# Optimization experiments

Measured on AMD Instinct MI355X. Metric: run time of the kernel, lower is better.

## Reference

```python
import jax, jax.numpy as jnp
import numpy as np

B, N, IN_DIM, SLOT_DIM, HIDDEN = 32, 4096, 256, 256, 512
NUM_SLOTS, NUM_ITERS = 8, 3
EPS_LN = 1e-5


def layernorm(x, g, b):
    m = jnp.mean(x, axis=-1, keepdims=True)
    v = jnp.var(x, axis=-1, keepdims=True)
    return (x - m) * jax.lax.rsqrt(v + EPS_LN) * g + b


def setup_inputs() -> dict:
    key = jax.random.key(0)
    ks = jax.random.split(key, 16)
    s = 0.02
    return {
        "inputs": jax.random.normal(ks[0], (B, N, IN_DIM), jnp.float32),
        "init_noise": jax.random.normal(ks[1], (B, NUM_SLOTS, SLOT_DIM), jnp.float32),
        "mu": jax.random.normal(ks[2], (1, 1, SLOT_DIM), jnp.float32),
        "sigma_raw": jax.random.normal(ks[3], (1, 1, SLOT_DIM), jnp.float32),
        "ln_in_g": jnp.ones((IN_DIM,), jnp.float32), "ln_in_b": jnp.zeros((IN_DIM,), jnp.float32),
        "ln_s_g": jnp.ones((SLOT_DIM,), jnp.float32), "ln_s_b": jnp.zeros((SLOT_DIM,), jnp.float32),
        "ln_m_g": jnp.ones((SLOT_DIM,), jnp.float32), "ln_m_b": jnp.zeros((SLOT_DIM,), jnp.float32),
        "wq": jax.random.normal(ks[4], (SLOT_DIM, SLOT_DIM), jnp.float32) * s,
        "bq": jnp.zeros((SLOT_DIM,), jnp.float32),
        "wk": jax.random.normal(ks[5], (SLOT_DIM, IN_DIM), jnp.float32) * s,
        "bk": jnp.zeros((SLOT_DIM,), jnp.float32),
        "wv": jax.random.normal(ks[6], (SLOT_DIM, IN_DIM), jnp.float32) * s,
        "bv": jnp.zeros((SLOT_DIM,), jnp.float32),
        "w_ih": jax.random.normal(ks[7], (3 * SLOT_DIM, SLOT_DIM), jnp.float32) * s,
        "w_hh": jax.random.normal(ks[8], (3 * SLOT_DIM, SLOT_DIM), jnp.float32) * s,
        "b_ih": jnp.zeros((3 * SLOT_DIM,), jnp.float32),
        "b_hh": jnp.zeros((3 * SLOT_DIM,), jnp.float32),
        "w1": jax.random.normal(ks[9], (HIDDEN, SLOT_DIM), jnp.float32) * s,
        "b1": jnp.zeros((HIDDEN,), jnp.float32),
        "w2": jax.random.normal(ks[10], (SLOT_DIM, HIDDEN), jnp.float32) * s,
        "b2": jnp.zeros((SLOT_DIM,), jnp.float32),
    }


def gru_cell(x, h, w_ih, w_hh, b_ih, b_hh):
    # PyTorch GRUCell: gates split as (reset, update, new)
    gx = x @ w_ih.T + b_ih
    gh = h @ w_hh.T + b_hh
    xr, xz, xn = jnp.split(gx, 3, axis=-1)
    hr, hz, hn = jnp.split(gh, 3, axis=-1)
    r = jax.nn.sigmoid(xr + hr)
    z = jax.nn.sigmoid(xz + hz)
    n = jnp.tanh(xn + r * hn)
    return (1.0 - z) * n + z * h


def reference(inputs, init_noise, mu, sigma_raw, ln_in_g, ln_in_b, ln_s_g, ln_s_b,
              ln_m_g, ln_m_b, wq, bq, wk, bk, wv, bv, w_ih, w_hh, b_ih, b_hh,
              w1, b1, w2, b2):
    scale = SLOT_DIM ** (-0.5)
    x = layernorm(inputs, ln_in_g, ln_in_b)          # [B,N,Din]
    k = x @ wk.T + bk                                # [B,N,D]
    v = x @ wv.T + bv                                # [B,N,D]
    sigma = jax.nn.softplus(sigma_raw)
    slots = mu + sigma * init_noise                  # [B,S,D]
    attn = None
    for _ in range(NUM_ITERS):
        slots_prev = slots
        q = layernorm(slots, ln_s_g, ln_s_b) @ wq.T + bq      # [B,S,D]
        logits = jnp.einsum('bnd,bsd->bns', k, q) * scale     # [B,N,S]
        attn = jax.nn.softmax(logits, axis=-1) + 1e-8         # softmax over slots
        attn = attn / jnp.sum(attn, axis=1, keepdims=True)    # renorm over inputs
        updates = jnp.einsum('bnd,bns->bsd', v, attn)         # [B,S,D]
        slots = gru_cell(updates, slots_prev, w_ih, w_hh, b_ih, b_hh)
        h = jax.nn.relu(layernorm(slots, ln_m_g, ln_m_b) @ w1.T + b1)
        slots = slots + (h @ w2.T + b2)
    return slots, attn
```

## Files before the change

kernel.cpp:

```cpp
#include <hip/hip_runtime.h>
#include <hip/hip_fp16.h>
#include <cstdint>

#define DEV static __device__ __forceinline__

typedef _Float16 f16x2 __attribute__((ext_vector_type(2)));
typedef _Float16 f16x8 __attribute__((ext_vector_type(8)));
typedef float    f32x4 __attribute__((ext_vector_type(4)));

DEV float fdot2u(uint32_t a, uint32_t b, float c){
  union U { uint32_t u; f16x2 h; };
  U ua; ua.u = a; U ub; ub.u = b;
#if __has_builtin(__builtin_amdgcn_fdot2)
  return __builtin_amdgcn_fdot2(ua.h, ub.h, c, false);
#else
  return c + (float)ua.h[0]*(float)ub.h[0] + (float)ua.h[1]*(float)ub.h[1];
#endif
}

DEV float dot4(uint4 x, uint4 w, float a){
  a = fdot2u(x.x, w.x, a); a = fdot2u(x.y, w.y, a);
  a = fdot2u(x.z, w.z, a); a = fdot2u(x.w, w.w, a);
  return a;
}

DEV float wsum64(float v){
  #pragma unroll
  for (int o = 32; o; o >>= 1) v += __shfl_xor(v, o);
  return v;
}

DEV uint32_t pack2h(float a, float b){
  __half ha = __float2half(a), hb = __float2half(b);
  return (uint32_t)__half_as_ushort(ha) | ((uint32_t)__half_as_ushort(hb) << 16);
}

DEV uint32_t packsh(float v){
  float o = __shfl_xor(v, 1);
  return pack2h(v, o);
}

DEV uint4 packrow8(const float* p){
  uint4 r;
  r.x = pack2h(p[0], p[1]); r.y = pack2h(p[2], p[3]);
  r.z = pack2h(p[4], p[5]); r.w = pack2h(p[6], p[7]);
  return r;
}

DEV void gld16(const void* g, void* l){
  __builtin_amdgcn_global_load_lds(
      (const __attribute__((address_space(1))) void*)g,
      (__attribute__((address_space(3))) void*)l, 16, 0, 0);
}

__global__ __launch_bounds__(256) void k_lntr(
  const float* __restrict__ xin, const float* __restrict__ lng,
  const float* __restrict__ lnb, uint32_t* __restrict__ xhat,
  const float* __restrict__ wq, const float* __restrict__ wv,
  const float* __restrict__ wih, const float* __restrict__ whh,
  const float* __restrict__ w1, const float* __restrict__ w2,
  const float* __restrict__ wk,
  uint4* __restrict__ WQp4, uint4* __restrict__ WVp4,
  uint4* __restrict__ WIHp4, uint4* __restrict__ WHHp4,
  uint4* __restrict__ W1p4, uint4* __restrict__ W2p4,
  uint4* __restrict__ WKp4)
{
  if (blockIdx.x >= 32768){
    int u = (blockIdx.x - 32768) * 256 + threadIdx.x;
    if (u < 8192){
      int e4 = u >> 8, n = u & 255;
      WVp4[u] = packrow8(wv + n*256 + 8*e4);
    } else if (u < 32768){
      int v = u - 8192; int e4 = v / 768, n = v - e4*768;
      WIHp4[v] = packrow8(wih + n*256 + 8*e4);
    } else if (u < 57344){
      int v = u - 32768; int e4 = v / 768, n = v - e4*768;
      WHHp4[v] = packrow8(whh + n*256 + 8*e4);
    } else if (u < 73728){
      int v = u - 57344; int e4 = v >> 9, n = v & 511;
      W1p4[v] = packrow8(w1 + n*256 + 8*e4);
    } else if (u < 90112){
      int v = u - 73728; int e4 = v >> 8, n = v & 255;
      W2p4[v] = packrow8(w2 + n*512 + 8*e4);
    } else if (u < 98304){
      int v = u - 90112; int e4 = v >> 8, n = v & 255;
      WQp4[v] = packrow8(wq + n*256 + 8*e4);
    } else if (u < 106496){
      int v = u - 98304; int d4 = v >> 8, c = v & 255;
      uint4 r;
      r.x = pack2h(wk[(8*d4+0)*256 + c], wk[(8*d4+1)*256 + c]);
      r.y = pack2h(wk[(8*d4+2)*256 + c], wk[(8*d4+3)*256 + c]);
      r.z = pack2h(wk[(8*d4+4)*256 + c], wk[(8*d4+5)*256 + c]);
      r.w = pack2h(wk[(8*d4+6)*256 + c], wk[(8*d4+7)*256 + c]);
      WKp4[v] = r;
    }
    return;
  }
  int row = blockIdx.x * 4 + (threadIdx.x >> 6);
  int lane = threadIdx.x & 63;
  const float4 xv = ((const float4*)(xin + (size_t)row * 256))[lane];
  float s1 = wsum64(xv.x + xv.y + xv.z + xv.w);
  float s2 = wsum64(xv.x*xv.x + xv.y*xv.y + xv.z*xv.z + xv.w*xv.w);
  float m = s1 * (1.0f/256.0f);
  float var = s2 * (1.0f/256.0f) - m*m;
  float rstd = rsqrtf(var + 1e-5f);
  float4 gv = ((const float4*)lng)[lane];
  float4 bv = ((const float4*)lnb)[lane];
  float y0 = (xv.x - m)*rstd*gv.x + bv.x;
  float y1 = (xv.y - m)*rstd*gv.y + bv.y;
  float y2 = (xv.z - m)*rstd*gv.z + bv.z;
  float y3 = (xv.w - m)*rstd*gv.w + bv.w;
  ((uint2*)(xhat + (size_t)row * 128))[lane] = make_uint2(pack2h(y0,y1), pack2h(y2,y3));
}

template<int MODE>
__global__ __launch_bounds__(512) void k_slot(
  const float* __restrict__ noise, const float* __restrict__ mu,
  const float* __restrict__ sigraw,
  const float* S0, float* SDST,
  const float* __restrict__ UAp, const float* __restrict__ ASp,
  float* __restrict__ OUTA,
  const uint4* __restrict__ WVp4, const float* __restrict__ bv,
  const uint4* __restrict__ WIHp4, const uint4* __restrict__ WHHp4,
  const float* __restrict__ bih, const float* __restrict__ bhh,
  const float* __restrict__ lmg, const float* __restrict__ lmb,
  const uint4* __restrict__ W1p4, const float* __restrict__ b1,
  const uint4* __restrict__ W2p4, const float* __restrict__ b2,
  const float* __restrict__ lsg, const float* __restrict__ lsb,
  const uint4* __restrict__ WQp4, const float* __restrict__ bq,
  const uint4* __restrict__ WKp4, const float* __restrict__ bk,
  uint32_t* __restrict__ QTH, float* __restrict__ CV)
{
  __shared__ float gx[768], gh[768];
  __shared__ float part[512];
  __shared__ uint4 hs4[32], un4[32], us4[32], sln4[32], q4[32];
  __shared__ uint4 hb4[64];
  __shared__ float redA[8], redB[8];
  __shared__ float asb[8];

  const int t = threadIdx.x;
  const int h = t >> 8;
  const int c = t & 255;
  const int lane = t & 63;
  const int w8 = t >> 6;
  const int r = blockIdx.x;
  const int b = r >> 3, s = r & 7;

  float snv = 0.f, spv = 0.f;

  if (MODE == 0){
    if (t < 256){
      float x = sigraw[c];
      float sp = (x > 20.0f) ? x : log1pf(__expf(x));
      snv = mu[c] + sp * noise[r*256 + c];
      SDST[r*256 + c] = snv;
    }
  } else {
    if (MODE == 2){
      if (lane < 16){
        float v = ASp[lane*256 + b*8 + w8];
        v += __shfl_xor(v, 1); v += __shfl_xor(v, 2);
        v += __shfl_xor(v, 4); v += __shfl_xor(v, 8);
        if (lane == 0) asb[w8] = v;
      }
    } else {
      if (w8 == 0){
        float v = (lane < 16) ? ASp[lane*256 + r] : 0.f;
        v += __shfl_xor(v, 1); v += __shfl_xor(v, 2);
        v += __shfl_xor(v, 4); v += __shfl_xor(v, 8);
        if (lane == 0) redA[0] = v;
      }
    }
    __syncthreads();
    const float asum_r = (MODE == 2) ? asb[s] : redA[0];
    const float ainv = 1.0f / asum_r;
    float hv = 0.f;
    if (t < 256){
      hv = S0[r*256 + c];
      float us = 0.f;
      #pragma unroll
      for (int ch = 0; ch < 16; ++ch) us += UAp[ch*65536 + r*256 + c];
      float unv = us * ainv;
      uint32_t ph = packsh(hv), pu = packsh(unv);
      if (!(c & 1)){
        ((uint32_t*)hs4)[c>>1] = ph;
        ((uint32_t*)un4)[c>>1] = pu;
      }
    }
    __syncthreads();

    {
      float a = 0.f;
      #pragma unroll 8
      for (int e4 = h*16; e4 < h*16 + 16; ++e4)
        a = dot4(un4[e4], WVp4[e4*256 + c], a);
      part[t] = a;
    }
    __syncthreads();
    if (t < 256){
      float us = part[t] + part[t + 256] + bv[c];
      uint32_t p = packsh(us);
      if (!(c & 1)) ((uint32_t*)us4)[c>>1] = p;
    }
    __syncthreads();

    {
      const uint4* IN4 = h ? hs4 : us4;
      const uint4* WP = h ? WHHp4 : WIHp4;
      float a0 = 0.f, a1 = 0.f, a2 = 0.f;
      #pragma unroll 8
      for (int e4 = 0; e4 < 32; ++e4){
        uint4 x = IN4[e4];
        a0 = dot4(x, WP[e4*768 + c], a0);
        a1 = dot4(x, WP[e4*768 + 256 + c], a1);
        a2 = dot4(x, WP[e4*768 + 512 + c], a2);
      }
      float* OUT = h ? gh : gx;
      OUT[c] = a0; OUT[256 + c] = a1; OUT[512 + c] = a2;
    }
    __syncthreads();

    if (t < 256){
      float xr = gx[c]     + bih[c];
      float xz = gx[256+c] + bih[256+c];
      float xn = gx[512+c] + bih[512+c];
      float hr = gh[c]     + bhh[c];
      float hz = gh[256+c] + bhh[256+c];
      float hn = gh[512+c] + bhh[512+c];
      float rg = 1.f/(1.f + __expf(-(xr + hr)));
      float zg = 1.f/(1.f + __expf(-(xz + hz)));
      float ng = tanhf(xn + rg*hn);
      spv = (1.f - zg)*ng + zg*hv;
      float a = wsum64(spv), bs = wsum64(spv*spv);
      if (lane == 0){ redA[w8] = a; redB[w8] = bs; }
    }
    __syncthreads();
    {
      float s1 = redA[0]+redA[1]+redA[2]+redA[3];
      float s2 = redB[0]+redB[1]+redB[2]+redB[3];
      float m = s1*(1.f/256.f), var = s2*(1.f/256.f) - m*m;
      float rstd = rsqrtf(var + 1e-5f);
      if (t < 256){
        float slv = (spv - m)*rstd*lmg[c] + lmb[c];
        uint32_t p = packsh(slv);
        if (!(c & 1)) ((uint32_t*)sln4)[c>>1] = p;
      }
    }
    __syncthreads();

    {
      float a = 0.f;
      #pragma unroll 8
      for (int e4 = 0; e4 < 32; ++e4)
        a = dot4(sln4[e4], W1p4[e4*512 + t], a);
      float hval = fmaxf(a + b1[t], 0.f);
      float o = __shfl_xor(hval, 1);
      if (!(t & 1)) ((uint32_t*)hb4)[t>>1] = pack2h(hval, o);
    }
    __syncthreads();

    {
      float a = 0.f;
      #pragma unroll 8
      for (int e4 = h*32; e4 < h*32 + 32; ++e4)
        a = dot4(hb4[e4], W2p4[e4*256 + c], a);
      part[t] = a;
    }
    __syncthreads();
    if (t < 256){
      snv = spv + part[t] + part[t + 256] + b2[c];
      SDST[r*256 + c] = snv;
    }
  }

  if (MODE != 2){
    if (t < 256){
      float a = wsum64(snv), bs = wsum64(snv*snv);
      if (lane == 0){ redA[w8] = a; redB[w8] = bs; }
    }
    __syncthreads();
    {
      float s1 = redA[0]+redA[1]+redA[2]+redA[3];
      float s2 = redB[0]+redB[1]+redB[2]+redB[3];
      float m = s1*(1.f/256.f), var = s2*(1.f/256.f) - m*m;
      float rstd = rsqrtf(var + 1e-5f);
      if (t < 256){
        float slv = (snv - m)*rstd*lsg[c] + lsb[c];
        uint32_t p = packsh(slv);
        if (!(c & 1)) ((uint32_t*)sln4)[c>>1] = p;
      }
    }
    __syncthreads();

    {
      float a = 0.f;
      #pragma unroll 8
      for (int e4 = h*16; e4 < h*16 + 16; ++e4)
        a = dot4(sln4[e4], WQp4[e4*256 + c], a);
      part[t] = a;
    }
    __syncthreads();
    if (t < 256){
      float qv = part[t] + part[t + 256] + bq[c];
      float p = wsum64(bk[c] * qv);
      if (lane == 0) redA[w8] = p;
      uint32_t pk = packsh(qv);
      if (!(c & 1)) ((uint32_t*)q4)[c>>1] = pk;
    }
    __syncthreads();
    {
      float cv = redA[0]+redA[1]+redA[2]+redA[3];
      if (t == 0) CV[r] = cv;
    }

    {
      float a = 0.f;
      #pragma unroll 8
      for (int e4 = h*16; e4 < h*16 + 16; ++e4)
        a = dot4(q4[e4], WKp4[e4*256 + c], a);
      part[t] = a;
    }
    __syncthreads();
    if (t < 256){
      float qtv = part[t] + part[t + 256];
      uint32_t p = packsh(qtv);
      if (!(c & 1)) QTH[b*1024 + (c>>1)*8 + s] = p;
    }
  } else if (s == 0){
    float inv[8];
    #pragma unroll
    for (int j = 0; j < 8; ++j) inv[j] = 1.0f / asb[j];
    float4* ap = (float4*)(OUTA + (size_t)b * 32768);
    #pragma unroll 4
    for (int i = t; i < 8192; i += 512){
      float4 v = ap[i];
      int h4 = (i & 1) * 4;
      v.x *= inv[h4+0]; v.y *= inv[h4+1]; v.z *= inv[h4+2]; v.w *= inv[h4+3];
      ap[i] = v;
    }
  }
}

template<bool LAST>
__global__ __launch_bounds__(256) void k_attn(
  const uint32_t* __restrict__ xhat,
  const uint32_t* __restrict__ qtpk, const float* __restrict__ cvec,
  float* __restrict__ UAp, float* __restrict__ ASp,
  float* __restrict__ attn_out)
{
  __shared__ __align__(16) uint32_t xs[2][8192];
  __shared__ uint32_t qs[1024];
  __shared__ float attn_lds[64][16];
  __shared__ float as_red[4][8];
  float* up_lds = (float*)&xs[0][0];

  const int b = blockIdx.y, chunk = blockIdx.x;
  const int t = threadIdx.x;
  const int l = t & 63, w = t >> 6;
  const int g = l >> 4, sl = l & 15;

  const size_t base = (size_t)b*4096 + (size_t)chunk*256;

  for (int i = t; i < 1024; i += 256) qs[i] = qtpk[b*1024 + i];

  auto stage = [&](int st){
    uint32_t* dst = &xs[st & 1][0];
    const size_t gr0 = base + (size_t)st*64;
    #pragma unroll
    for (int i = 0; i < 8; ++i){
      int n  = w*8 + i;
      int rl = 2*n + (l >> 5);
      int ql = (l & 31) ^ (rl & 7);
      gld16(xhat + (gr0 + rl)*128 + ql*4, dst + n*256);
    }
  };

  stage(0);
  __syncthreads();

  uint4 bq[8];
  #pragma unroll
  for (int kk = 0; kk < 8; ++kk){
    if (sl < 8){
      uint4 v;
      v.x = qs[(16*kk + 4*g + 0)*8 + sl];
      v.y = qs[(16*kk + 4*g + 1)*8 + sl];
      v.z = qs[(16*kk + 4*g + 2)*8 + sl];
      v.w = qs[(16*kk + 4*g + 3)*8 + sl];
      bq[kk] = v;
    } else bq[kk] = make_uint4(0u,0u,0u,0u);
  }
  const float cv = (sl < 8) ? cvec[b*8 + sl] : 0.f;

  float up[8][4];
  #pragma unroll
  for (int s = 0; s < 8; ++s){ up[s][0]=0.f; up[s][1]=0.f; up[s][2]=0.f; up[s][3]=0.f; }
  float asl_acc = 0.f;

  for (int st = 0; st < 4; ++st){
    if (st) __syncthreads();
    if (st < 3) stage(st + 1);
    const uint32_t* xb = &xs[st & 1][0];
    const int L0 = 16*w;

    f32x4 acc; acc[0]=0.f; acc[1]=0.f; acc[2]=0.f; acc[3]=0.f;
    const int rowA = L0 + sl;
    #pragma unroll
    for (int kk = 0; kk < 8; ++kk){
      uint4 av = *(const uint4*)(xb + rowA*128 + (((4*kk + g) ^ (rowA & 7)) << 2));
      union { uint4 u; f16x8 h; } A, B;
      A.u = av; B.u = bq[kk];
      acc = __builtin_amdgcn_mfma_f32_16x16x32_f16(A.h, B.h, acc, 0, 0, 0);
    }

    #pragma unroll
    for (int reg = 0; reg < 4; ++reg){
      float d = (acc[reg] + cv) * 0.0625f;
      float m = d;
      m = fmaxf(m, __shfl_xor(m, 1));
      m = fmaxf(m, __shfl_xor(m, 2));
      m = fmaxf(m, __shfl_xor(m, 4));
      float e = __expf(d - m);
      float ssum = e;
      ssum += __shfl_xor(ssum, 1);
      ssum += __shfl_xor(ssum, 2);
      ssum += __shfl_xor(ssum, 4);
      float a = e / ssum + 1e-8f;
      asl_acc += a;
      attn_lds[L0 + 4*g + reg][sl] = a;
    }

    #pragma unroll 4
    for (int rr = 0; rr < 16; ++rr){
      const int row = L0 + rr;
      const uint32_t* xp = xb + row*128 + ((((l>>1) ^ (row & 7)) << 2) | ((l & 1) << 1));
      uint2 xv = *(const uint2*)xp;
      float x0 = __half2float(__ushort_as_half((unsigned short)(xv.x & 0xffff)));
      float x1 = __half2float(__ushort_as_half((unsigned short)(xv.x >> 16)));
      float x2 = __half2float(__ushort_as_half((unsigned short)(xv.y & 0xffff)));
      float x3 = __half2float(__ushort_as_half((unsigned short)(xv.y >> 16)));
      const float4 a0 = *(const float4*)&attn_lds[row][0];
      const float4 a1 = *(const float4*)&attn_lds[row][4];
      float as8[8] = {a0.x, a0.y, a0.z, a0.w, a1.x, a1.y, a1.z, a1.w};
      #pragma unroll
      for (int s = 0; s < 8; ++s){
        up[s][0] += as8[s]*x0; up[s][1] += as8[s]*x1;
        up[s][2] += as8[s]*x2; up[s][3] += as8[s]*x3;
      }
    }

    if (LAST){
      __syncthreads();
      int row = t >> 2, s0 = (t & 3)*2;
      float2 v = *(const float2*)&attn_lds[row][s0];
      *(float2*)(attn_out + (base + (size_t)st*64 + row)*8 + s0) = v;
    }
  }

  {
    float v = asl_acc;
    v += __shfl_xor(v, 16);
    v += __shfl_xor(v, 32);
    if (l < 8) as_red[w][l] = v;
  }

  __syncthreads();
  #pragma unroll
  for (int ww = 0; ww < 4; ++ww){
    if (w == ww){
      #pragma unroll
      for (int s = 0; s < 8; ++s){
        float4* dst = (float4*)&up_lds[s*256 + l*4];
        float4 v = make_float4(up[s][0], up[s][1], up[s][2], up[s][3]);
        if (ww){ float4 o = *dst; v.x += o.x; v.y += o.y; v.z += o.z; v.w += o.w; }
        *dst = v;
      }
    }
    __syncthreads();
  }
  #pragma unroll
  for (int s = 0; s < 8; ++s)
    UAp[(size_t)chunk*65536 + (size_t)(b*8 + s)*256 + t] = up_lds[s*256 + t];
  if (t < 8)
    ASp[chunk*256 + b*8 + t] = as_red[0][t] + as_red[1][t] + as_red[2][t] + as_red[3][t];
}

extern "C" void kernel_launch(void* const* d_in, const int* in_sizes, int n_in,
                              void* d_out, int out_size, void* d_ws, size_t ws_size,
                              hipStream_t stream) {
  const float* inputs = (const float*)d_in[0];
  const float* noise  = (const float*)d_in[1];
  const float* mu     = (const float*)d_in[2];
  const float* sigraw = (const float*)d_in[3];
  const float* lng    = (const float*)d_in[4];
  const float* lnb    = (const float*)d_in[5];
  const float* lsg    = (const float*)d_in[6];
  const float* lsb    = (const float*)d_in[7];
  const float* lmg    = (const float*)d_in[8];
  const float* lmb    = (const float*)d_in[9];
  const float* wq     = (const float*)d_in[10];
  const float* bq     = (const float*)d_in[11];
  const float* wk     = (const float*)d_in[12];
  const float* bk     = (const float*)d_in[13];
  const float* wv     = (const float*)d_in[14];
  const float* bv     = (const float*)d_in[15];
  const float* wih    = (const float*)d_in[16];
  const float* whh    = (const float*)d_in[17];
  const float* bih    = (const float*)d_in[18];
  const float* bhh    = (const float*)d_in[19];
  const float* w1     = (const float*)d_in[20];
  const float* b1     = (const float*)d_in[21];
  const float* w2     = (const float*)d_in[22];
  const float* b2     = (const float*)d_in[23];
  float* out = (float*)d_out;

  char* w = (char*)d_ws;
  size_t o = 0;
  uint32_t* XH = (uint32_t*)w;  o += 67108864;
  uint32_t* QT = (uint32_t*)(w + o); o += 131072;
  float* CV  = (float*)(w + o); o += 1024;
  float* S0  = (float*)(w + o); o += 262144;
  uint4* WQp = (uint4*)(w + o); o += 131072;
  uint4* WVp = (uint4*)(w + o); o += 131072;
  uint4* WIHp= (uint4*)(w + o); o += 393216;
  uint4* WHHp= (uint4*)(w + o); o += 393216;
  uint4* W1p = (uint4*)(w + o); o += 262144;
  uint4* W2p = (uint4*)(w + o); o += 262144;
  uint4* WKp = (uint4*)(w + o); o += 131072;
  float* UAp = (float*)(w + o); o += 4194304;
  float* ASp = (float*)(w + o); o += 16384;

  float* OUTA = out + 65536;

  k_lntr<<<33184, 256, 0, stream>>>(inputs, lng, lnb, XH,
                                    wq, wv, wih, whh, w1, w2, wk,
                                    WQp, WVp, WIHp, WHHp, W1p, W2p, WKp);
  k_slot<0><<<256, 512, 0, stream>>>(noise, mu, sigraw, S0, S0, UAp, ASp, OUTA,
      WVp, bv, WIHp, WHHp, bih, bhh, lmg, lmb, W1p, b1, W2p, b2,
      lsg, lsb, WQp, bq, WKp, bk, QT, CV);

  dim3 ga(16, 32);
  for (int it = 0; it < 3; ++it){
    if (it == 2) k_attn<true ><<<ga, 256, 0, stream>>>(XH, QT, CV, UAp, ASp, OUTA);
    else         k_attn<false><<<ga, 256, 0, stream>>>(XH, QT, CV, UAp, ASp, OUTA);
    if (it < 2)
      k_slot<1><<<256, 512, 0, stream>>>(noise, mu, sigraw, S0, S0, UAp, ASp, OUTA,
          WVp, bv, WIHp, WHHp, bih, bhh, lmg, lmb, W1p, b1, W2p, b2,
          lsg, lsb, WQp, bq, WKp, bk, QT, CV);
    else
      k_slot<2><<<256, 512, 0, stream>>>(noise, mu, sigraw, S0, out, UAp, ASp, OUTA,
          WVp, bv, WIHp, WHHp, bih, bhh, lmg, lmb, W1p, b1, W2p, b2,
          lsg, lsb, WQp, bq, WKp, bk, QT, CV);
  }
}
```

Measured before the change: 377.3 us.

## Fuse all stages into one cooperative persistent kernel with grid syncs

Replaces the sequence of separate launches (layernorm/repack, slot init, three attention passes and slot updates) with a single cooperative kernel of 256 blocks × 512 threads, separated by grid.sync barriers. Shared memory is a union reused across phases, each block runs two attention chunks side by side, and the final attention renormalisation is spread over all slot blocks instead of one per batch. This aims to remove launch and inter-kernel gaps. The cost is that the layernorm pass now runs on only 256 blocks looping over rows, and grid-wide barriers cap occupancy.

After: 1.128 ms. 199% more time.

```diff
diff --git a/kernel.cpp b/kernel.cpp
--- a/kernel.cpp
+++ b/kernel.cpp
@@ -1,6 +1,9 @@
 #include <hip/hip_runtime.h>
 #include <hip/hip_fp16.h>
+#include <hip/hip_cooperative_groups.h>
 #include <cstdint>
+
+namespace cg = cooperative_groups;
 
 #define DEV static __device__ __forceinline__
 
@@ -53,138 +56,138 @@
       (__attribute__((address_space(3))) void*)l, 16, 0, 0);
 }
 
-__global__ __launch_bounds__(256) void k_lntr(
-  const float* __restrict__ xin, const float* __restrict__ lng,
-  const float* __restrict__ lnb, uint32_t* __restrict__ xhat,
-  const float* __restrict__ wq, const float* __restrict__ wv,
-  const float* __restrict__ wih, const float* __restrict__ whh,
-  const float* __restrict__ w1, const float* __restrict__ w2,
-  const float* __restrict__ wk,
-  uint4* __restrict__ WQp4, uint4* __restrict__ WVp4,
-  uint4* __restrict__ WIHp4, uint4* __restrict__ WHHp4,
-  uint4* __restrict__ W1p4, uint4* __restrict__ W2p4,
-  uint4* __restrict__ WKp4)
-{
-  if (blockIdx.x >= 32768){
-    int u = (blockIdx.x - 32768) * 256 + threadIdx.x;
+struct MegaParams {
+  const float *xin, *lng, *lnb;
+  const float *noise, *mu, *sigraw;
+  const float *lsg, *lsb, *lmg, *lmb;
+  const float *wq, *bq, *wk, *bk, *wv, *bv;
+  const float *wih, *whh, *bih, *bhh;
+  const float *w1, *b1, *w2, *b2;
+  uint32_t *XH;
+  uint32_t *QT;
+  float *CV;
+  float *S0;
+  uint4 *WQp, *WVp, *WIHp, *WHHp, *W1p, *W2p, *WKp;
+  float *UAp;
+  float *ASp;
+  float *out;
+};
+
+struct AttnSh {
+  uint32_t xs[2][2][8192];
+  uint32_t qs[1024];
+  float attn_lds[2][64][16];
+  float as_red[2][4][8];
+};
+struct SlotSh {
+  float gx[768], gh[768], part[512];
+  uint4 hs4[32], un4[32], us4[32], sln4[32], q4[32];
+  uint4 hb4[64];
+  float redA[8], redB[8], asb[8];
+};
+union MegaSh { AttnSh a; SlotSh s; };
+
+DEV void ln_repack(const MegaParams& P, int bid, int t){
+  int gid = bid*512 + t;
+  if (gid < 106496){
+    int u = gid;
     if (u < 8192){
       int e4 = u >> 8, n = u & 255;
-      WVp4[u] = packrow8(wv + n*256 + 8*e4);
+      P.WVp[u] = packrow8(P.wv + n*256 + 8*e4);
     } else if (u < 32768){
       int v = u - 8192; int e4 = v / 768, n = v - e4*768;
-      WIHp4[v] = packrow8(wih + n*256 + 8*e4);
+      P.WIHp[v] = packrow8(P.wih + n*256 + 8*e4);
     } else if (u < 57344){
       int v = u - 32768; int e4 = v / 768, n = v - e4*768;
-      WHHp4[v] = packrow8(whh + n*256 + 8*e4);
+      P.WHHp[v] = packrow8(P.whh + n*256 + 8*e4);
     } else if (u < 73728){
       int v = u - 57344; int e4 = v >> 9, n = v & 511;
-      W1p4[v] = packrow8(w1 + n*256 + 8*e4);
+      P.W1p[v] = packrow8(P.w1 + n*256 + 8*e4);
     } else if (u < 90112){
       int v = u - 73728; int e4 = v >> 8, n = v & 255;
-      W2p4[v] = packrow8(w2 + n*512 + 8*e4);
+      P.W2p[v] = packrow8(P.w2 + n*512 + 8*e4);
     } else if (u < 98304){
       int v = u - 90112; int e4 = v >> 8, n = v & 255;
-      WQp4[v] = packrow8(wq + n*256 + 8*e4);
-    } else if (u < 106496){
+      P.WQp[v] = packrow8(P.wq + n*256 + 8*e4);
+    } else {
       int v = u - 98304; int d4 = v >> 8, c = v & 255;
       uint4 r;
-      r.x = pack2h(wk[(8*d4+0)*256 + c], wk[(8*d4+1)*256 + c]);
-      r.y = pack2h(wk[(8*d4+2)*256 + c], wk[(8*d4+3)*256 + c]);
-      r.z = pack2h(wk[(8*d4+4)*256 + c], wk[(8*d4+5)*256 + c]);
-      r.w = pack2h(wk[(8*d4+6)*256 + c], wk[(8*d4+7)*256 + c]);
-      WKp4[v] = r;
-    }
-    return;
-  }
-  int row = blockIdx.x * 4 + (threadIdx.x >> 6);
-  int lane = threadIdx.x & 63;
-  const float4 xv = ((const float4*)(xin + (size_t)row * 256))[lane];
-  float s1 = wsum64(xv.x + xv.y + xv.z + xv.w);
-  float s2 = wsum64(xv.x*xv.x + xv.y*xv.y + xv.z*xv.z + xv.w*xv.w);
-  float m = s1 * (1.0f/256.0f);
-  float var = s2 * (1.0f/256.0f) - m*m;
-  float rstd = rsqrtf(var + 1e-5f);
-  float4 gv = ((const float4*)lng)[lane];
-  float4 bv = ((const float4*)lnb)[lane];
-  float y0 = (xv.x - m)*rstd*gv.x + bv.x;
-  float y1 = (xv.y - m)*rstd*gv.y + bv.y;
-  float y2 = (xv.z - m)*rstd*gv.z + bv.z;
-  float y3 = (xv.w - m)*rstd*gv.w + bv.w;
-  ((uint2*)(xhat + (size_t)row * 128))[lane] = make_uint2(pack2h(y0,y1), pack2h(y2,y3));
+      r.x = pack2h(P.wk[(8*d4+0)*256 + c], P.wk[(8*d4+1)*256 + c]);
+      r.y = pack2h(P.wk[(8*d4+2)*256 + c], P.wk[(8*d4+3)*256 + c]);
+      r.z = pack2h(P.wk[(8*d4+4)*256 + c], P.wk[(8*d4+5)*256 + c]);
+      r.w = pack2h(P.wk[(8*d4+6)*256 + c], P.wk[(8*d4+7)*256 + c]);
+      P.WKp[v] = r;
+    }
+  }
+  const int w8 = t >> 6, lane = t & 63;
+  const int rbase = bid * 512;
+  const float4 gv = ((const float4*)P.lng)[lane];
+  const float4 bv = ((const float4*)P.lnb)[lane];
+  #pragma unroll 2
+  for (int i = 0; i < 64; ++i){
+    int row = rbase + i*8 + w8;
+    const float4 xv = ((const float4*)(P.xin + (size_t)row * 256))[lane];
+    float s1 = wsum64(xv.x + xv.y + xv.z + xv.w);
+    float s2 = wsum64(xv.x*xv.x + xv.y*xv.y + xv.z*xv.z + xv.w*xv.w);
+    float m = s1 * (1.0f/256.0f);
+    float var = s2 * (1.0f/256.0f) - m*m;
+    float rstd = rsqrtf(var + 1e-5f);
+    float y0 = (xv.x - m)*rstd*gv.x + bv.x;
+    float y1 = (xv.y - m)*rstd*gv.y + bv.y;
+    float y2 = (xv.z - m)*rstd*gv.z + bv.z;
+    float y3 = (xv.w - m)*rstd*gv.w + bv.w;
+    ((uint2*)(P.XH + (size_t)row * 128))[lane] = make_uint2(pack2h(y0,y1), pack2h(y2,y3));
+  }
 }
 
 template<int MODE>
-__global__ __launch_bounds__(512) void k_slot(
-  const float* __restrict__ noise, const float* __restrict__ mu,
-  const float* __restrict__ sigraw,
-  const float* S0, float* SDST,
-  const float* __restrict__ UAp, const float* __restrict__ ASp,
-  float* __restrict__ OUTA,
-  const uint4* __restrict__ WVp4, const float* __restrict__ bv,
-  const uint4* __restrict__ WIHp4, const uint4* __restrict__ WHHp4,
-  const float* __restrict__ bih, const float* __restrict__ bhh,
-  const float* __restrict__ lmg, const float* __restrict__ lmb,
-  const uint4* __restrict__ W1p4, const float* __restrict__ b1,
-  const uint4* __restrict__ W2p4, const float* __restrict__ b2,
-  const float* __restrict__ lsg, const float* __restrict__ lsb,
-  const uint4* __restrict__ WQp4, const float* __restrict__ bq,
-  const uint4* __restrict__ WKp4, const float* __restrict__ bk,
-  uint32_t* __restrict__ QTH, float* __restrict__ CV)
-{
-  __shared__ float gx[768], gh[768];
-  __shared__ float part[512];
-  __shared__ uint4 hs4[32], un4[32], us4[32], sln4[32], q4[32];
-  __shared__ uint4 hb4[64];
-  __shared__ float redA[8], redB[8];
-  __shared__ float asb[8];
-
-  const int t = threadIdx.x;
+DEV void slot_phase(const MegaParams& P, SlotSh& ss, int r, int t){
   const int h = t >> 8;
   const int c = t & 255;
   const int lane = t & 63;
   const int w8 = t >> 6;
-  const int r = blockIdx.x;
   const int b = r >> 3, s = r & 7;
+  float* SDST = (MODE == 2) ? P.out : P.S0;
 
   float snv = 0.f, spv = 0.f;
 
   if (MODE == 0){
     if (t < 256){
-      float x = sigraw[c];
+      float x = P.sigraw[c];
       float sp = (x > 20.0f) ? x : log1pf(__expf(x));
-      snv = mu[c] + sp * noise[r*256 + c];
+      snv = P.mu[c] + sp * P.noise[r*256 + c];
       SDST[r*256 + c] = snv;
     }
   } else {
     if (MODE == 2){
       if (lane < 16){
-        float v = ASp[lane*256 + b*8 + w8];
+        float v = P.ASp[lane*256 + b*8 + w8];
         v += __shfl_xor(v, 1); v += __shfl_xor(v, 2);
         v += __shfl_xor(v, 4); v += __shfl_xor(v, 8);
-        if (lane == 0) asb[w8] = v;
+        if (lane == 0) ss.asb[w8] = v;
       }
     } else {
       if (w8 == 0){
-        float v = (lane < 16) ? ASp[lane*256 + r] : 0.f;
+        float v = (lane < 16) ? P.ASp[lane*256 + r] : 0.f;
         v += __shfl_xor(v, 1); v += __shfl_xor(v, 2);
         v += __shfl_xor(v, 4); v += __shfl_xor(v, 8);
-        if (lane == 0) redA[0] = v;
-      }
-    }
-    __syncthreads();
-    const float asum_r = (MODE == 2) ? asb[s] : redA[0];
+        if (lane == 0) ss.redA[0] = v;
+      }
+    }
+    __syncthreads();
+    const float asum_r = (MODE == 2) ? ss.asb[s] : ss.redA[0];
     const float ainv = 1.0f / asum_r;
     float hv = 0.f;
     if (t < 256){
-      hv = S0[r*256 + c];
+      hv = P.S0[r*256 + c];
       float us = 0.f;
       #pragma unroll
-      for (int ch = 0; ch < 16; ++ch) us += UAp[ch*65536 + r*256 + c];
+      for (int ch = 0; ch < 16; ++ch) us += P.UAp[ch*65536 + r*256 + c];
       float unv = us * ainv;
       uint32_t ph = packsh(hv), pu = packsh(unv);
       if (!(c & 1)){
-        ((uint32_t*)hs4)[c>>1] = ph;
-        ((uint32_t*)un4)[c>>1] = pu;
+        ((uint32_t*)ss.hs4)[c>>1] = ph;
+        ((uint32_t*)ss.un4)[c>>1] = pu;
       }
     }
     __syncthreads();
@@ -193,20 +196,20 @@
       float a = 0.f;
       #pragma unroll 8
       for (int e4 = h*16; e4 < h*16 + 16; ++e4)
-        a = dot4(un4[e4], WVp4[e4*256 + c], a);
-      part[t] = a;
-    }
-    __syncthreads();
-    if (t < 256){
-      float us = part[t] + part[t + 256] + bv[c];
+        a = dot4(ss.un4[e4], P.WVp[e4*256 + c], a);
+      ss.part[t] = a;
+    }
+    __syncthreads();
+    if (t < 256){
+      float us = ss.part[t] + ss.part[t + 256] + P.bv[c];
       uint32_t p = packsh(us);
-      if (!(c & 1)) ((uint32_t*)us4)[c>>1] = p;
-    }
-    __syncthreads();
-
-    {
-      const uint4* IN4 = h ? hs4 : us4;
-      const uint4* WP = h ? WHHp4 : WIHp4;
+      if (!(c & 1)) ((uint32_t*)ss.us4)[c>>1] = p;
+    }
+    __syncthreads();
+
+    {
+      const uint4* IN4 = h ? ss.hs4 : ss.us4;
+      const uint4* WP = h ? P.WHHp : P.WIHp;
       float a0 = 0.f, a1 = 0.f, a2 = 0.f;
       #pragma unroll 8
       for (int e4 = 0; e4 < 32; ++e4){
@@ -215,35 +218,35 @@
         a1 = dot4(x, WP[e4*768 + 256 + c], a1);
         a2 = dot4(x, WP[e4*768 + 512 + c], a2);
       }
-      float* OUT = h ? gh : gx;
+      float* OUT = h ? ss.gh : ss.gx;
       OUT[c] = a0; OUT[256 + c] = a1; OUT[512 + c] = a2;
     }
     __syncthreads();
 
     if (t < 256){
-      float xr = gx[c]     + bih[c];
-      float xz = gx[256+c] + bih[256+c];
-      float xn = gx[512+c] + bih[512+c];
-      float hr = gh[c]     + bhh[c];
-      float hz = gh[256+c] + bhh[256+c];
-      float hn = gh[512+c] + bhh[512+c];
+      float xr = ss.gx[c]     + P.bih[c];
+      float xz = ss.gx[256+c] + P.bih[256+c];
+      float xn = ss.gx[512+c] + P.bih[512+c];
+      float hr = ss.gh[c]     + P.bhh[c];
+      float hz = ss.gh[256+c] + P.bhh[256+c];
+      float hn = ss.gh[512+c] + P.bhh[512+c];
       float rg = 1.f/(1.f + __expf(-(xr + hr)));
       float zg = 1.f/(1.f + __expf(-(xz + hz)));
       float ng = tanhf(xn + rg*hn);
       spv = (1.f - zg)*ng + zg*hv;
       float a = wsum64(spv), bs = wsum64(spv*spv);
-      if (lane == 0){ redA[w8] = a; redB[w8] = bs; }
-    }
-    __syncthreads();
-    {
-      float s1 = redA[0]+redA[1]+redA[2]+redA[3];
-      float s2 = redB[0]+redB[1]+redB[2]+redB[3];
+      if (lane == 0){ ss.redA[w8] = a; ss.redB[w8] = bs; }
+    }
+    __syncthreads();
+    {
+      float s1 = ss.redA[0]+ss.redA[1]+ss.redA[2]+ss.redA[3];
+      float s2 = ss.redB[0]+ss.redB[1]+ss.redB[2]+ss.redB[3];
       float m = s1*(1.f/256.f), var = s2*(1.f/256.f) - m*m;
       float rstd = rsqrtf(var + 1e-5f);
       if (t < 256){
-        float slv = (spv - m)*rstd*lmg[c] + lmb[c];
+        float slv = (spv - m)*rstd*P.lmg[c] + P.lmb[c];
         uint32_t p = packsh(slv);
-        if (!(c & 1)) ((uint32_t*)sln4)[c>>1] = p;
+        if (!(c & 1)) ((uint32_t*)ss.sln4)[c>>1] = p;
       }
     }
     __syncthreads();
@@ -252,10 +255,10 @@
       float a = 0.f;
       #pragma unroll 8
       for (int e4 = 0; e4 < 32; ++e4)
-        a = dot4(sln4[e4], W1p4[e4*512 + t], a);
-      float hval = fmaxf(a + b1[t], 0.f);
+        a = dot4(ss.sln4[e4], P.W1p[e4*512 + t], a);
+      float hval = fmaxf(a + P.b1[t], 0.f);
       float o = __shfl_xor(hval, 1);
-      if (!(t & 1)) ((uint32_t*)hb4)[t>>1] = pack2h(hval, o);
+      if (!(t & 1)) ((uint32_t*)ss.hb4)[t>>1] = pack2h(hval, o);
     }
     __syncthreads();
 
@@ -263,12 +266,12 @@
       float a = 0.f;
       #pragma unroll 8
       for (int e4 = h*32; e4 < h*32 + 32; ++e4)
-        a = dot4(hb4[e4], W2p4[e4*256 + c], a);
-      part[t] = a;
-    }
-    __syncthreads();
-    if (t < 256){
-      snv = spv + part[t] + part[t + 256] + b2[c];
+        a = dot4(ss.hb4[e4], P.W2p[e4*256 + c], a);
+      ss.part[t] = a;
+    }
+    __syncthreads();
+    if (t < 256){
+      snv = spv + ss.part[t] + ss.part[t + 256] + P.b2[c];
       SDST[r*256 + c] = snv;
     }
   }
@@ -276,18 +279,18 @@
   if (MODE != 2){
     if (t < 256){
       float a = wsum64(snv), bs = wsum64(snv*snv);
-      if (lane == 0){ redA[w8] = a; redB[w8] = bs; }
-    }
-    __syncthreads();
-    {
-      float s1 = redA[0]+redA[1]+redA[2]+redA[3];
-      float s2 = redB[0]+redB[1]+redB[2]+redB[3];
+      if (lane == 0){ ss.redA[w8] = a; ss.redB[w8] = bs; }
+    }
+    __syncthreads();
+    {
+      float s1 = ss.redA[0]+ss.redA[1]+ss.redA[2]+ss.redA[3];
+      float s2 = ss.redB[0]+ss.redB[1]+ss.redB[2]+ss.redB[3];
       float m = s1*(1.f/256.f), var = s2*(1.f/256.f) - m*m;
       float rstd = rsqrtf(var + 1e-5f);
       if (t < 256){
-        float slv = (snv - m)*rstd*lsg[c] + lsb[c];
+        float slv = (snv - m)*rstd*P.lsg[c] + P.lsb[c];
         uint32_t p = packsh(slv);
-        if (!(c & 1)) ((uint32_t*)sln4)[c>>1] = p;
+        if (!(c & 1)) ((uint32_t*)ss.sln4)[c>>1] = p;
       }
     }
     __syncthreads();
@@ -296,82 +299,80 @@
       float a = 0.f;
       #pragma unroll 8
       for (int e4 = h*16; e4 < h*16 + 16; ++e4)
-        a = dot4(sln4[e4], WQp4[e4*256 + c], a);
-      part[t] = a;
-    }
-    __syncthreads();
-    if (t < 256){
-      float qv = part[t] + part[t + 256] + bq[c];
-      float p = wsum64(bk[c] * qv);
-      if (lane == 0) redA[w8] = p;
+        a = dot4(ss.sln4[e4], P.WQp[e4*256 + c], a);
+      ss.part[t] = a;
+    }
+    __syncthreads();
+    if (t < 256){
+      float qv = ss.part[t] + ss.part[t + 256] + P.bq[c];
+      float p = wsum64(P.bk[c] * qv);
+      if (lane == 0) ss.redA[w8] = p;
       uint32_t pk = packsh(qv);
-      if (!(c & 1)) ((uint32_t*)q4)[c>>1] = pk;
-    }
-    __syncthreads();
-    {
-      float cv = redA[0]+redA[1]+redA[2]+redA[3];
-      if (t == 0) CV[r] = cv;
+      if (!(c & 1)) ((uint32_t*)ss.q4)[c>>1] = pk;
+    }
+    __syncthreads();
+    {
+      float cv = ss.redA[0]+ss.redA[1]+ss.redA[2]+ss.redA[3];
+      if (t == 0) P.CV[r] = cv;
     }
 
     {
       float a = 0.f;
       #pragma unroll 8
       for (int e4 = h*16; e4 < h*16 + 16; ++e4)
-        a = dot4(q4[e4], WKp4[e4*256 + c], a);
-      part[t] = a;
-    }
-    __syncthreads();
-    if (t < 256){
-      float qtv = part[t] + part[t + 256];
+        a = dot4(ss.q4[e4], P.WKp[e4*256 + c], a);
+      ss.part[t] = a;
+    }
+    __syncthreads();
+    if (t < 256){
+      float qtv = ss.part[t] + ss.part[t + 256];
       uint32_t p = packsh(qtv);
-      if (!(c & 1)) QTH[b*1024 + (c>>1)*8 + s] = p;
-    }
-  } else if (s == 0){
+      if (!(c & 1)) P.QT[b*1024 + (c>>1)*8 + s] = p;
+    }
+  } else {
     float inv[8];
     #pragma unroll
-    for (int j = 0; j < 8; ++j) inv[j] = 1.0f / asb[j];
-    float4* ap = (float4*)(OUTA + (size_t)b * 32768);
-    #pragma unroll 4
-    for (int i = t; i < 8192; i += 512){
-      float4 v = ap[i];
-      int h4 = (i & 1) * 4;
+    for (int j = 0; j < 8; ++j) inv[j] = 1.0f / ss.asb[j];
+    float4* ap = (float4*)(P.out + 65536 + (size_t)b * 32768);
+    #pragma unroll
+    for (int i = t; i < 1024; i += 512){
+      int idx = s*1024 + i;
+      float4 v = ap[idx];
+      int h4 = (idx & 1) * 4;
       v.x *= inv[h4+0]; v.y *= inv[h4+1]; v.z *= inv[h4+2]; v.w *= inv[h4+3];
-      ap[i] = v;
+      ap[idx] = v;
     }
   }
 }
 
 template<bool LAST>
-__global__ __launch_bounds__(256) void k_attn(
-  const uint32_t* __restrict__ xhat,
-  const uint32_t* __restrict__ qtpk, const float* __restrict__ cvec,
-  float* __restrict__ UAp, float* __restrict__ ASp,
-  float* __restrict__ attn_out)
-{
-  __shared__ __align__(16) uint32_t xs[2][8192];
-  __shared__ uint32_t qs[1024];
-  __shared__ float attn_lds[64][16];
-  __shared__ float as_red[4][8];
-  float* up_lds = (float*)&xs[0][0];
-
-  const int b = blockIdx.y, chunk = blockIdx.x;
-  const int t = threadIdx.x;
-  const int l = t & 63, w = t >> 6;
+DEV void attn_phase(const MegaParams& P, AttnSh& A, int bid, int t){
+  const int gg = t >> 8;
+  const int tg = t & 255;
+  const int l  = t & 63;
+  const int wl = (t >> 6) & 3;
   const int g = l >> 4, sl = l & 15;
 
+  const int b = bid >> 3;
+  const int chunk = ((bid & 7) << 1) | gg;
   const size_t base = (size_t)b*4096 + (size_t)chunk*256;
 
-  for (int i = t; i < 1024; i += 256) qs[i] = qtpk[b*1024 + i];
+  uint32_t* xs0 = &A.xs[gg][0][0];
+  uint32_t* xs1 = &A.xs[gg][1][0];
+  float (*attn_lds)[16] = A.attn_lds[gg];
+  float* up_lds = (float*)xs0;
+
+  for (int i = t; i < 1024; i += 512) A.qs[i] = P.QT[b*1024 + i];
 
   auto stage = [&](int st){
-    uint32_t* dst = &xs[st & 1][0];
+    uint32_t* dst = (st & 1) ? xs1 : xs0;
     const size_t gr0 = base + (size_t)st*64;
     #pragma unroll
     for (int i = 0; i < 8; ++i){
-      int n  = w*8 + i;
+      int n  = wl*8 + i;
       int rl = 2*n + (l >> 5);
       int ql = (l & 31) ^ (rl & 7);
-      gld16(xhat + (gr0 + rl)*128 + ql*4, dst + n*256);
+      gld16(P.XH + (gr0 + rl)*128 + ql*4, dst + n*256);
     }
   };
 
@@ -383,14 +384,14 @@
   for (int kk = 0; kk < 8; ++kk){
     if (sl < 8){
       uint4 v;
-      v.x = qs[(16*kk + 4*g + 0)*8 + sl];
-      v.y = qs[(16*kk + 4*g + 1)*8 + sl];
-      v.z = qs[(16*kk + 4*g + 2)*8 + sl];
-      v.w = qs[(16*kk + 4*g + 3)*8 + sl];
+      v.x = A.qs[(16*kk + 4*g + 0)*8 + sl];
+      v.y = A.qs[(16*kk + 4*g + 1)*8 + sl];
+      v.z = A.qs[(16*kk + 4*g + 2)*8 + sl];
+      v.w = A.qs[(16*kk + 4*g + 3)*8 + sl];
       bq[kk] = v;
     } else bq[kk] = make_uint4(0u,0u,0u,0u);
   }
-  const float cv = (sl < 8) ? cvec[b*8 + sl] : 0.f;
+  const float cv = (sl < 8) ? P.CV[b*8 + sl] : 0.f;
 
   float up[8][4];
   #pragma unroll
@@ -400,17 +401,17 @@
   for (int st = 0; st < 4; ++st){
     if (st) __syncthreads();
     if (st < 3) stage(st + 1);
-    const uint32_t* xb = &xs[st & 1][0];
-    const int L0 = 16*w;
+    const uint32_t* xb = (st & 1) ? xs1 : xs0;
+    const int L0 = 16*wl;
 
     f32x4 acc; acc[0]=0.f; acc[1]=0.f; acc[2]=0.f; acc[3]=0.f;
     const int rowA = L0 + sl;
     #pragma unroll
     for (int kk = 0; kk < 8; ++kk){
       uint4 av = *(const uint4*)(xb + rowA*128 + (((4*kk + g) ^ (rowA & 7)) << 2));
-      union { uint4 u; f16x8 h; } A, B;
-      A.u = av; B.u = bq[kk];
-      acc = __builtin_amdgcn_mfma_f32_16x16x32_f16(A.h, B.h, acc, 0, 0, 0);
+      union { uint4 u; f16x8 h; } Au, Bu;
+      Au.u = av; Bu.u = bq[kk];
+      acc = __builtin_amdgcn_mfma_f32_16x16x32_f16(Au.h, Bu.h, acc, 0, 0, 0);
     }
 
     #pragma unroll
@@ -451,9 +452,9 @@
 
     if (LAST){
       __syncthreads();
-      int row = t >> 2, s0 = (t & 3)*2;
+      int row = tg >> 2, s0 = (tg & 3)*2;
       float2 v = *(const float2*)&attn_lds[row][s0];
-      *(float2*)(attn_out + (base + (size_t)st*64 + row)*8 + s0) = v;
+      *(float2*)(P.out + 65536 + (base + (size_t)st*64 + row)*8 + s0) = v;
     }
   }
 
@@ -461,13 +462,13 @@
     float v = asl_acc;
     v += __shfl_xor(v, 16);
     v += __shfl_xor(v, 32);
-    if (l < 8) as_red[w][l] = v;
+    if (l < 8) A.as_red[gg][wl][l] = v;
   }
 
   __syncthreads();
   #pragma unroll
   for (int ww = 0; ww < 4; ++ww){
-    if (w == ww){
+    if (wl == ww){
       #pragma unroll
       for (int s = 0; s < 8; ++s){
         float4* dst = (float4*)&up_lds[s*256 + l*4];
@@ -480,9 +481,39 @@
   }
   #pragma unroll
   for (int s = 0; s < 8; ++s)
-    UAp[(size_t)chunk*65536 + (size_t)(b*8 + s)*256 + t] = up_lds[s*256 + t];
-  if (t < 8)
-    ASp[chunk*256 + b*8 + t] = as_red[0][t] + as_red[1][t] + as_red[2][t] + as_red[3][t];
+    P.UAp[(size_t)chunk*65536 + (size_t)(b*8 + s)*256 + tg] = up_lds[s*256 + tg];
+  if (tg < 8)
+    P.ASp[chunk*256 + b*8 + tg] =
+      A.as_red[gg][0][tg] + A.as_red[gg][1][tg] + A.as_red[gg][2][tg] + A.as_red[gg][3][tg];
+}
+
+__global__ __launch_bounds__(512, 2) void k_mega(MegaParams P){
+  cg::grid_group grid = cg::this_grid();
+  __shared__ MegaSh SH;
+  const int bid = blockIdx.x;
+  const int t = threadIdx.x;
+
+  ln_repack(P, bid, t);
+  __threadfence();
+  grid.sync();
+
+  slot_phase<0>(P, SH.s, bid, t);
+  __threadfence();
+  grid.sync();
+
+  for (int it = 0; it < 3; ++it){
+    if (it == 2) attn_phase<true >(P, SH.a, bid, t);
+    else         attn_phase<false>(P, SH.a, bid, t);
+    __threadfence();
+    grid.sync();
+    if (it < 2){
+      slot_phase<1>(P, SH.s, bid, t);
+      __threadfence();
+      grid.sync();
+    } else {
+      slot_phase<2>(P, SH.s, bid, t);
+    }
+  }
 }
 
 extern "C" void kernel_launch(void* const* d_in, const int* in_sizes, int n_in,
@@ -530,26 +561,18 @@
   float* UAp = (float*)(w + o); o += 4194304;
   float* ASp = (float*)(w + o); o += 16384;
 
-  float* OUTA = out + 65536;
-
-  k_lntr<<<33184, 256, 0, stream>>>(inputs, lng, lnb, XH,
-                                    wq, wv, wih, whh, w1, w2, wk,
-                                    WQp, WVp, WIHp, WHHp, W1p, W2p, WKp);
-  k_slot<0><<<256, 512, 0, stream>>>(noise, mu, sigraw, S0, S0, UAp, ASp, OUTA,
-      WVp, bv, WIHp, WHHp, bih, bhh, lmg, lmb, W1p, b1, W2p, b2,
-      lsg, lsb, WQp, bq, WKp, bk, QT, CV);
-
-  dim3 ga(16, 32);
-  for (int it = 0; it < 3; ++it){
-    if (it == 2) k_attn<true ><<<ga, 256, 0, stream>>>(XH, QT, CV, UAp, ASp, OUTA);
-    else         k_attn<false><<<ga, 256, 0, stream>>>(XH, QT, CV, UAp, ASp, OUTA);
-    if (it < 2)
-      k_slot<1><<<256, 512, 0, stream>>>(noise, mu, sigraw, S0, S0, UAp, ASp, OUTA,
-          WVp, bv, WIHp, WHHp, bih, bhh, lmg, lmb, W1p, b1, W2p, b2,
-          lsg, lsb, WQp, bq, WKp, bk, QT, CV);
-    else
-      k_slot<2><<<256, 512, 0, stream>>>(noise, mu, sigraw, S0, out, UAp, ASp, OUTA,
-          WVp, bv, WIHp, WHHp, bih, bhh, lmg, lmb, W1p, b1, W2p, b2,
-          lsg, lsb, WQp, bq, WKp, bk, QT, CV);
-  }
-}
+  MegaParams mp;
+  mp.xin = inputs; mp.lng = lng; mp.lnb = lnb;
+  mp.noise = noise; mp.mu = mu; mp.sigraw = sigraw;
+  mp.lsg = lsg; mp.lsb = lsb; mp.lmg = lmg; mp.lmb = lmb;
+  mp.wq = wq; mp.bq = bq; mp.wk = wk; mp.bk = bk; mp.wv = wv; mp.bv = bv;
+  mp.wih = wih; mp.whh = whh; mp.bih = bih; mp.bhh = bhh;
+  mp.w1 = w1; mp.b1 = b1; mp.w2 = w2; mp.b2 = b2;
+  mp.XH = XH; mp.QT = QT; mp.CV = CV; mp.S0 = S0;
+  mp.WQp = WQp; mp.WVp = WVp; mp.WIHp = WIHp; mp.WHHp = WHHp;
+  mp.W1p = W1p; mp.W2p = W2p; mp.WKp = WKp;
+  mp.UAp = UAp; mp.ASp = ASp; mp.out = out;
+
+  void* args[] = { (void*)&mp };
+  hipLaunchCooperativeKernel((const void*)k_mega, dim3(256), dim3(512), args, 0, stream);
+}
```
